# Kernel tuning notes

Measured on AMD Instinct MI355X. Metric: run time of the kernel, lower is better.

## Reference

```python
import jax, jax.numpy as jnp
import numpy as np

COST_CLASS, COST_BBOX, COST_GIOU = 2.0, 5.0, 2.0
ALPHA, GAMMA = 0.25, 2.0
EPS = 1e-8
N_CANDIDATE = 10


def box_cxcywh_to_xyxy(b):
    cx, cy, w, h = b[..., 0], b[..., 1], b[..., 2], b[..., 3]
    return jnp.stack([cx - 0.5 * w, cy - 0.5 * h, cx + 0.5 * w, cy + 0.5 * h], axis=-1)


def pairwise_iou_giou(b1, b2):
    # b1: [N,4] xyxy, b2: [M,4] xyxy -> iou [N,M], giou [N,M]
    area1 = (b1[:, 2] - b1[:, 0]) * (b1[:, 3] - b1[:, 1])
    area2 = (b2[:, 2] - b2[:, 0]) * (b2[:, 3] - b2[:, 1])
    lt = jnp.maximum(b1[:, None, :2], b2[None, :, :2])
    rb = jnp.minimum(b1[:, None, 2:], b2[None, :, 2:])
    wh = jnp.clip(rb - lt, 0.0)
    inter = wh[..., 0] * wh[..., 1]
    union = area1[:, None] + area2[None, :] - inter
    iou = inter / (union + EPS)
    # smallest enclosing box
    lt_c = jnp.minimum(b1[:, None, :2], b2[None, :, :2])
    rb_c = jnp.maximum(b1[:, None, 2:], b2[None, :, 2:])
    wh_c = jnp.clip(rb_c - lt_c, 0.0)
    area_c = wh_c[..., 0] * wh_c[..., 1]
    giou = iou - (area_c - union) / (area_c + EPS)
    return iou, giou


def _match_one(logits, boxes, labels, tboxes):
    # logits [Q,C], boxes [Q,4] cxcywh, labels [G] int, tboxes [G,4] cxcywh
    Q = logits.shape[0]
    G = labels.shape[0]
    prob = jax.nn.sigmoid(logits)                 # [Q,C]  (use_focal_loss path)
    p = prob[:, labels]                           # [Q,G] gather at GT classes
    neg_cost = (1.0 - ALPHA) * p ** GAMMA * (-jnp.log1p(-p + EPS))
    pos_cost = ALPHA * (1.0 - p) ** GAMMA * (-jnp.log(p + EPS))
    cost_class = pos_cost - neg_cost              # [Q,G]
    cost_bbox = jnp.sum(jnp.abs(boxes[:, None, :] - tboxes[None, :, :]), axis=-1)  # L1 cdist [Q,G]
    iou, giou = pairwise_iou_giou(box_cxcywh_to_xyxy(boxes), box_cxcywh_to_xyxy(tboxes))
    C = COST_BBOX * cost_bbox + COST_CLASS * cost_class + COST_GIOU * (-giou)      # [Q,G]

    # --- SimOTA matching (simota_matching), vectorized over GT ---
    cost = C.T                                    # [G,Q]
    ious = iou.T                                  # [G,Q]
    n_cand = min(N_CANDIDATE, Q)
    topk_ious, _ = jax.lax.top_k(ious, n_cand)    # [G,n_cand]
    dynamic_ks = jnp.clip(jnp.sum(topk_ious, axis=1).astype(jnp.int32), 1)  # [G]
    # rank of each anchor per GT under ascending cost
    ranks = jnp.argsort(jnp.argsort(cost, axis=1), axis=1)                  # [G,Q]
    matching = (ranks < dynamic_ks[:, None]).astype(cost.dtype)             # [G,Q]
    # resolve anchors matched to multiple GTs: keep argmin-cost GT
    anchor_matching_gt = matching.sum(axis=0)     # [Q]
    cost_argmin = jnp.argmin(cost, axis=0)        # [Q]
    onehot_min = (jnp.arange(G)[:, None] == cost_argmin[None, :]).astype(cost.dtype)
    matching = jnp.where(anchor_matching_gt[None, :] > 1, onehot_min, matching)
    return jnp.stack([cost, matching], axis=0)    # [2,G,Q]


def reference(pred_logits, pred_boxes, tgt_labels, tgt_boxes):
    # per-image cost blocks + SimOTA matching matrices: [bs, 2, G, Q]
    return jax.vmap(_match_one)(pred_logits, pred_boxes, tgt_labels, tgt_boxes)


def setup_inputs() -> dict:
    key = jax.random.key(0)
    k1, k2, k3, k4 = jax.random.split(key, 4)
    bs, Q, C, G = 16, 4000, 80, 128
    pred_logits = jax.random.normal(k1, (bs, Q, C), dtype=jnp.float32)
    pred_boxes = jax.random.uniform(k2, (bs, Q, 4), dtype=jnp.float32, minval=0.05, maxval=0.95)
    tgt_labels = jax.random.randint(k3, (bs, G), 0, C)
    tgt_boxes = jax.random.uniform(k4, (bs, G, 4), dtype=jnp.float32, minval=0.05, maxval=0.95)
    return {"pred_logits": pred_logits, "pred_boxes": pred_boxes,
            "tgt_labels": tgt_labels, "tgt_boxes": tgt_boxes}
```

## Files before the change

kernel.cpp:

```cpp
#include <hip/hip_runtime.h>
#include <cmath>
#include <cfloat>
#include <climits>


static constexpr int BS = 16;
static constexpr int Qn = 4000;
static constexpr int Cn = 80;
static constexpr int Gn = 128;
static constexpr float kEPS = 1e-8f;


static constexpr size_t kThrvOff = 0;
static constexpr size_t kThriOff = 8 * 1024;
static constexpr size_t kFOff    = 16 * 1024;
static constexpr size_t kFBytes  = (size_t)BS * Cn * Qn * sizeof(float);

__device__ __forceinline__ float focal_cost(float l) {
    const float p = 1.0f / (1.0f + expf(-l));
    const float neg = (0.75f * (p * p)) * (-log1pf(-p + kEPS));
    const float pos = (0.25f * ((1.0f - p) * (1.0f - p))) * (-logf(p + kEPS));
    return pos - neg;
}

__global__ __launch_bounds__(256) void kP_focal(
    const float* __restrict__ logits,
    float* __restrict__ F)
{
    const int b  = blockIdx.y;
    const int q0 = blockIdx.x * 32;
    const int t  = threadIdx.x;

    __shared__ float s_f[32 * 81];

    const float* src = logits + ((size_t)b * Qn + q0) * Cn;
#pragma unroll
    for (int i = 0; i < 10; ++i) {
        const int idx = t + i * 256;
        const int ql = idx / 80, c = idx % 80;
        s_f[ql * 81 + c] = focal_cost(src[idx]);
    }
    __syncthreads();

    float* dst = F + (size_t)b * Cn * Qn;
#pragma unroll
    for (int i = 0; i < 10; ++i) {
        const int j = t + i * 256;
        const int c = j >> 5, ql = j & 31;
        dst[(size_t)c * Qn + q0 + ql] = s_f[ql * 81 + c];
    }
}

__device__ __forceinline__ unsigned long long pack_ci(float c, int q) {
    const unsigned int u = __float_as_uint(c + 0.0f);
    const unsigned int s = (u & 0x80000000u) ? ~u : (u | 0x80000000u);
    return ((unsigned long long)s << 32) | (unsigned int)q;
}

__device__ __forceinline__ unsigned long long shfl_xor_u64(unsigned long long v, int m) {
    const int lo = __shfl_xor((int)(unsigned int)v, m, 64);
    const int hi = __shfl_xor((int)(unsigned int)(v >> 32), m, 64);
    return ((unsigned long long)(unsigned int)hi << 32) | (unsigned int)lo;
}

__device__ __forceinline__ unsigned long long bitonic64_asc_u64(unsigned long long v, int lane) {
#pragma unroll
    for (int k = 2; k <= 64; k <<= 1) {
#pragma unroll
        for (int j = 32; j >= 1; j >>= 1) {
            if (j < k) {
                const unsigned long long o = shfl_xor_u64(v, j);
                const bool up = ((lane & k) == 0);
                const bool keepmin = (((lane & j) == 0) == up);
                const bool omin = (o < v);
                v = (keepmin == omin) ? o : v;
            }
        }
    }
    return v;
}

__device__ __forceinline__ float bitonic64_asc_f32(float v, int lane) {
#pragma unroll
    for (int k = 2; k <= 64; k <<= 1) {
#pragma unroll
        for (int j = 32; j >= 1; j >>= 1) {
            if (j < k) {
                const float o = __shfl_xor(v, j, 64);
                const bool up = ((lane & k) == 0);
                const bool keepmin = (((lane & j) == 0) == up);
                const bool omin = (o < v);
                v = (keepmin == omin) ? o : v;
            }
        }
    }
    return v;
}

__device__ __forceinline__ void ins10_vi(float (&cv)[10], int (&ci)[10],
                                         float v, int q) {
    bool le[10];
#pragma unroll
    for (int j = 0; j < 10; ++j) le[j] = (cv[j] <= v);
#pragma unroll
    for (int j = 9; j >= 1; --j) {
        const float nv = le[j] ? cv[j] : (le[j - 1] ? v : cv[j - 1]);
        const int   ni = le[j] ? ci[j] : (le[j - 1] ? q : ci[j - 1]);
        cv[j] = nv; ci[j] = ni;
    }
    if (!le[0]) { cv[0] = v; ci[0] = q; }
}

__device__ __forceinline__ void ins10_desc(float (&iv)[10], float v) {
    bool ge[10];
#pragma unroll
    for (int j = 0; j < 10; ++j) ge[j] = (iv[j] >= v);
#pragma unroll
    for (int j = 9; j >= 1; --j)
        iv[j] = ge[j] ? iv[j] : (ge[j - 1] ? v : iv[j - 1]);
    if (!ge[0]) iv[0] = v;
}

template <bool USE_F>
__global__ __launch_bounds__(512, 8) void kF(
    const float* __restrict__ boxes,
    const int*   __restrict__ labels,
    const float* __restrict__ tboxes,
    const float* __restrict__ logits,
    const float* __restrict__ F,
    float* __restrict__ out,
    float* __restrict__ thrv,
    int*   __restrict__ thri)
{
    const int lane = threadIdx.x & 63;
    const int w8   = threadIdx.x >> 6;
    const int sub  = w8 & 3;
    const int r    = blockIdx.x;
    const int b    = r >> 7;
    const int g    = r & (Gn - 1);

    const float* tb = tboxes + (size_t)r * 4;
    const float tcx = tb[0], tcy = tb[1], tw = tb[2], th = tb[3];
    const float tx0 = tcx - 0.5f * tw, ty0 = tcy - 0.5f * th;
    const float tx1 = tcx + 0.5f * tw, ty1 = tcy + 0.5f * th;
    const float tarea = (tx1 - tx0) * (ty1 - ty0);

    const float4* brow = reinterpret_cast<const float4*>(boxes) + (size_t)b * Qn;

    __shared__ float              s_st[8][1024];
    __shared__ unsigned long long s_ccb[4][64];
    __shared__ float              s_icb[4][64];
    __shared__ int                s_cnt[8];
    __shared__ unsigned long long s_ce[4][12];
    __shared__ float              s_if[4][12];

    if (lane == 0) s_cnt[w8] = 0;

    if (w8 < 4) {
        const int lab = labels[r];
        const float* Frow = USE_F ? (F + ((size_t)b * Cn + lab) * Qn) : nullptr;
        const float* lcol = USE_F ? nullptr : (logits + (size_t)b * Qn * Cn + lab);
        float* crow = out + (size_t)(b * 2) * Gn * Qn + (size_t)g * Qn;

        float m0 = INFINITY;

#pragma unroll
        for (int it = 0; it < 4; ++it) {
            const int q0 = it * 1024 + sub * 256 + (lane << 2);
            if ((it < 3) || (q0 < Qn)) {
                float cls4[4];
                if (USE_F) {
                    const float4 f4 = *reinterpret_cast<const float4*>(Frow + q0);
                    cls4[0] = f4.x; cls4[1] = f4.y; cls4[2] = f4.z; cls4[3] = f4.w;
                } else {
#pragma unroll
                    for (int e = 0; e < 4; ++e)
                        cls4[e] = focal_cost(lcol[(size_t)(q0 + e) * Cn]);
                }
                float c4[4];
#pragma unroll
                for (int e = 0; e < 4; ++e) {
                    const float cls = cls4[e];
                    const float4 bb = brow[q0 + e];
                    const float cx = bb.x, cy = bb.y, w = bb.z, h = bb.w;
                    const float x0 = cx - 0.5f * w, y0 = cy - 0.5f * h;
                    const float x1 = cx + 0.5f * w, y1 = cy + 0.5f * h;
                    const float area1 = (x1 - x0) * (y1 - y0);
                    const float l1 = ((fabsf(cx - tcx) + fabsf(cy - tcy))
                                      + fabsf(w - tw)) + fabsf(h - th);
                    const float ltx = fmaxf(x0, tx0), lty = fmaxf(y0, ty0);
                    const float rbx = fminf(x1, tx1), rby = fminf(y1, ty1);
                    const float iw = fmaxf(rbx - ltx, 0.0f), ih = fmaxf(rby - lty, 0.0f);
                    const float inter = iw * ih;
                    const float uni = (area1 + tarea) - inter;
                    const float iou = inter / (uni + kEPS);
                    const float cltx = fminf(x0, tx0), clty = fminf(y0, ty0);
                    const float crbx = fmaxf(x1, tx1), crby = fmaxf(y1, ty1);
                    const float cw = fmaxf(crbx - cltx, 0.0f), ch = fmaxf(crby - clty, 0.0f);
                    const float areac = cw * ch;
                    const float giou = iou - (areac - uni) / (areac + kEPS);

                    const float cost = (5.0f * l1 + 2.0f * cls) + 2.0f * (-giou);
                    c4[e] = cost;
                    m0 = fminf(m0, cost);
                }
                float4 cv4; cv4.x = c4[0]; cv4.y = c4[1]; cv4.z = c4[2]; cv4.w = c4[3];
                *reinterpret_cast<float4*>(crow + q0) = cv4;
                *reinterpret_cast<float4*>(&s_st[w8][it * 256 + (lane << 2)]) = cv4;
            }
        }

        const float sorted = bitonic64_asc_f32(m0, lane);
        const float T = __shfl(sorted, 9, 64);

#pragma unroll
        for (int it = 0; it < 4; ++it) {
            const int q0 = it * 1024 + sub * 256 + (lane << 2);
            if ((it < 3) || (q0 < Qn)) {
                const float4 c4 = *reinterpret_cast<const float4*>(
                    &s_st[w8][it * 256 + (lane << 2)]);
#pragma unroll
                for (int e = 0; e < 4; ++e) {
                    const float c = (e == 0) ? c4.x : (e == 1) ? c4.y
                                  : (e == 2) ? c4.z : c4.w;
                    if (c <= T) {
                        const int slot = atomicAdd(&s_cnt[w8], 1);
                        if (slot < 64) s_ccb[sub][slot] = pack_ci(c, q0 + e);
                    }
                }
            }
        }

        const int cnt = s_cnt[w8];
        if (cnt <= 64) {
            unsigned long long v = (lane < cnt) ? s_ccb[sub][lane] : ~0ull;
            v = bitonic64_asc_u64(v, lane);
            if (lane < 12) s_ce[sub][lane] = (lane < 10) ? v : ~0ull;
        } else {
            float cv[10]; int ci[10];
#pragma unroll
            for (int j = 0; j < 10; ++j) { cv[j] = INFINITY; ci[j] = INT_MAX; }
#pragma unroll
            for (int it = 0; it < 4; ++it) {
                const int q0 = it * 1024 + sub * 256 + (lane << 2);
                if ((it < 3) || (q0 < Qn)) {
                    const float4 c4 = *reinterpret_cast<const float4*>(
                        &s_st[w8][it * 256 + (lane << 2)]);
                    ins10_vi(cv, ci, c4.x, q0);
                    ins10_vi(cv, ci, c4.y, q0 + 1);
                    ins10_vi(cv, ci, c4.z, q0 + 2);
                    ins10_vi(cv, ci, c4.w, q0 + 3);
                }
            }
#pragma unroll
            for (int t = 0; t < 10; ++t) {
                float m = cv[0];
#pragma unroll
                for (int d = 1; d <= 32; d <<= 1)
                    m = fminf(m, __shfl_xor(m, d, 64));
                int cq = (cv[0] == m) ? ci[0] : INT_MAX;
#pragma unroll
                for (int d = 1; d <= 32; d <<= 1)
                    cq = min(cq, __shfl_xor(cq, d, 64));
                if (lane == 0) s_ce[sub][t] = pack_ci(m, cq);
                const bool own = (cv[0] == m) && (ci[0] == cq);
                if (own) {
#pragma unroll
                    for (int j = 0; j < 9; ++j) { cv[j] = cv[j + 1]; ci[j] = ci[j + 1]; }
                    cv[9] = INFINITY; ci[9] = INT_MAX;
                }
            }
            if (lane < 2) s_ce[sub][10 + lane] = ~0ull;
        }
    } else {
        float M0 = -INFINITY;

#pragma unroll
        for (int it = 0; it < 4; ++it) {
            const int q0 = it * 1024 + sub * 256 + (lane << 2);
            if ((it < 3) || (q0 < Qn)) {
                float io4[4];
#pragma unroll
                for (int e = 0; e < 4; ++e) {
                    const float4 bb = brow[q0 + e];
                    const float x0 = bb.x - 0.5f * bb.z, y0 = bb.y - 0.5f * bb.w;
                    const float x1 = bb.x + 0.5f * bb.z, y1 = bb.y + 0.5f * bb.w;
                    const float area1 = (x1 - x0) * (y1 - y0);
                    const float ltx = fmaxf(x0, tx0), lty = fmaxf(y0, ty0);
                    const float rbx = fminf(x1, tx1), rby = fminf(y1, ty1);
                    const float iw = fmaxf(rbx - ltx, 0.0f), ih = fmaxf(rby - lty, 0.0f);
                    const float inter = iw * ih;
                    const float uni = (area1 + tarea) - inter;
                    const float iou = inter / (uni + kEPS);
                    io4[e] = iou;
                    M0 = fmaxf(M0, iou);
                }
                float4 iv4; iv4.x = io4[0]; iv4.y = io4[1]; iv4.z = io4[2]; iv4.w = io4[3];
                *reinterpret_cast<float4*>(&s_st[w8][it * 256 + (lane << 2)]) = iv4;
            }
        }

        const float sorted = bitonic64_asc_f32(M0, lane);
        const float T = __shfl(sorted, 54, 64);

#pragma unroll
        for (int it = 0; it < 4; ++it) {
            const int q0 = it * 1024 + sub * 256 + (lane << 2);
            if ((it < 3) || (q0 < Qn)) {
                const float4 c4 = *reinterpret_cast<const float4*>(
                    &s_st[w8][it * 256 + (lane << 2)]);
#pragma unroll
                for (int e = 0; e < 4; ++e) {
                    const float c = (e == 0) ? c4.x : (e == 1) ? c4.y
                                  : (e == 2) ? c4.z : c4.w;
                    if (c >= T) {
                        const int slot = atomicAdd(&s_cnt[w8], 1);
                        if (slot < 64) s_icb[sub][slot] = c;
                    }
                }
            }
        }

        const int cnt = s_cnt[w8];
        if (cnt <= 64) {
            float v = (lane < cnt) ? s_icb[sub][lane] : -INFINITY;
            v = bitonic64_asc_f32(v, lane);
            if (lane >= 54) s_if[sub][63 - lane] = v;
            if (lane < 2) s_if[sub][10 + lane] = -INFINITY;
        } else {
            float iv[10];
#pragma unroll
            for (int j = 0; j < 10; ++j) iv[j] = -INFINITY;
#pragma unroll
            for (int it = 0; it < 4; ++it) {
                const int q0 = it * 1024 + sub * 256 + (lane << 2);
                if ((it < 3) || (q0 < Qn)) {
                    const float4 c4 = *reinterpret_cast<const float4*>(
                        &s_st[w8][it * 256 + (lane << 2)]);
                    ins10_desc(iv, c4.x);
                    ins10_desc(iv, c4.y);
                    ins10_desc(iv, c4.z);
                    ins10_desc(iv, c4.w);
                }
            }
#pragma unroll
            for (int t = 0; t < 10; ++t) {
                float m = iv[0];
#pragma unroll
                for (int d = 1; d <= 32; d <<= 1)
                    m = fmaxf(m, __shfl_xor(m, d, 64));
                if (lane == 0) s_if[sub][t] = m;
                const bool own0 = (iv[0] == m);
                const unsigned long long bal = __ballot(own0);
                if (own0 && lane == __ffsll((long long)bal) - 1) {
#pragma unroll
                    for (int j = 0; j < 9; ++j) iv[j] = iv[j + 1];
                    iv[9] = -INFINITY;
                }
            }
            if (lane < 2) s_if[sub][10 + lane] = -INFINITY;
        }
    }

    __syncthreads();

    if (threadIdx.x == 0) {
        int p0 = 0, p1 = 0, p2 = 0, p3 = 0;
        float s = 0.0f;
#pragma unroll
        for (int t = 0; t < 10; ++t) {
            const float a0 = s_if[0][p0], a1 = s_if[1][p1];
            const float a2 = s_if[2][p2], a3 = s_if[3][p3];
            const float mx = fmaxf(fmaxf(a0, a1), fmaxf(a2, a3));
            if (a0 == mx) ++p0;
            else if (a1 == mx) ++p1;
            else if (a2 == mx) ++p2;
            else ++p3;
            s += mx;
        }
        int k = (int)s;
        if (k < 1) k = 1;
        if (k > 10) k = 10;

        p0 = 0; p1 = 0; p2 = 0; p3 = 0;
        unsigned long long key = 0;
#pragma unroll
        for (int t = 0; t < 10; ++t) {
            const unsigned long long a0 = s_ce[0][p0], a1 = s_ce[1][p1];
            const unsigned long long a2 = s_ce[2][p2], a3 = s_ce[3][p3];
            unsigned long long mn = a0;
            if (a1 < mn) mn = a1;
            if (a2 < mn) mn = a2;
            if (a3 < mn) mn = a3;
            if (a0 == mn) ++p0;
            else if (a1 == mn) ++p1;
            else if (a2 == mn) ++p2;
            else ++p3;
            if (t == k - 1) key = mn;
        }
        const unsigned int su = (unsigned int)(key >> 32);
        thrv[r] = __uint_as_float((su & 0x80000000u) ? (su ^ 0x80000000u) : ~su);
        thri[r] = (int)(unsigned int)key;
    }
}

__global__ __launch_bounds__(512) void kC5(
    const float* __restrict__ outc,
    const float* __restrict__ thrv,
    const int*   __restrict__ thri,
    float* __restrict__ out)
{
    const int b    = blockIdx.y;
    const int lane = threadIdx.x & 63;
    const int gh   = threadIdx.x >> 6;
    const int quad = blockIdx.x * 64 + lane;
    const int q0   = quad * 4;

    __shared__ float              s_tv[Gn];
    __shared__ int                s_ti[Gn];
    __shared__ unsigned long long s_mask[8][64];
    __shared__ float              s_mv0[8][64], s_mv1[8][64];
    __shared__ float              s_mv2[8][64], s_mv3[8][64];
    __shared__ unsigned           s_mg[8][64];

    if (threadIdx.x < Gn) {
        s_tv[threadIdx.x] = thrv[b * Gn + threadIdx.x];
        s_ti[threadIdx.x] = thri[b * Gn + threadIdx.x];
    }
    __syncthreads();

    const bool act = (quad < Qn / 4);
    const int gbase = gh * 16;
    unsigned long long mask = 0;
    float mv0 = INFINITY, mv1 = INFINITY, mv2 = INFINITY, mv3 = INFINITY;
    int mg0 = 0, mg1 = 0, mg2 = 0, mg3 = 0;

    if (act) {
        const float* crow = outc + (size_t)(b * 2) * Gn * Qn + q0;
#pragma unroll
        for (int j = 0; j < 16; ++j) {
            const int g = gbase + j;
            const float4 c = *reinterpret_cast<const float4*>(crow + (size_t)g * Qn);
            const float tvg = s_tv[g];
            const int   tig = s_ti[g];
            const bool t0 = (c.x < tvg) || (c.x == tvg && q0     <= tig);
            const bool t1 = (c.y < tvg) || (c.y == tvg && q0 + 1 <= tig);
            const bool t2 = (c.z < tvg) || (c.z == tvg && q0 + 2 <= tig);
            const bool t3 = (c.w < tvg) || (c.w == tvg && q0 + 3 <= tig);
            mask |= ((unsigned long long)t0 << j)
                  | ((unsigned long long)t1 << (16 + j))
                  | ((unsigned long long)t2 << (32 + j))
                  | ((unsigned long long)t3 << (48 + j));
            if (c.x < mv0) { mv0 = c.x; mg0 = g; }
            if (c.y < mv1) { mv1 = c.y; mg1 = g; }
            if (c.z < mv2) { mv2 = c.z; mg2 = g; }
            if (c.w < mv3) { mv3 = c.w; mg3 = g; }
        }
    }
    s_mask[gh][lane] = mask;
    s_mv0[gh][lane] = mv0; s_mv1[gh][lane] = mv1;
    s_mv2[gh][lane] = mv2; s_mv3[gh][lane] = mv3;
    s_mg[gh][lane] = (unsigned)mg0 | ((unsigned)mg1 << 8)
                   | ((unsigned)mg2 << 16) | ((unsigned)mg3 << 24);
    __syncthreads();

    int c0 = 0, c1 = 0, c2 = 0, c3 = 0;
#pragma unroll
    for (int h = 0; h < 8; ++h) {
        const unsigned long long m = s_mask[h][lane];
        c0 += __popcll(m & 0xFFFFull);
        c1 += __popcll((m >> 16) & 0xFFFFull);
        c2 += __popcll((m >> 32) & 0xFFFFull);
        c3 += __popcll((m >> 48) & 0xFFFFull);
    }
    float b0 = s_mv0[0][lane], b1 = s_mv1[0][lane];
    float b2 = s_mv2[0][lane], b3 = s_mv3[0][lane];
    unsigned pk = s_mg[0][lane];
    int g0b = pk & 0xFF, g1b = (pk >> 8) & 0xFF;
    int g2b = (pk >> 16) & 0xFF, g3b = (pk >> 24) & 0xFF;
#pragma unroll
    for (int h = 1; h < 8; ++h) {
        const unsigned pkh = s_mg[h][lane];
        const float v0 = s_mv0[h][lane];
        if (v0 < b0) { b0 = v0; g0b = pkh & 0xFF; }
        const float v1 = s_mv1[h][lane];
        if (v1 < b1) { b1 = v1; g1b = (pkh >> 8) & 0xFF; }
        const float v2 = s_mv2[h][lane];
        if (v2 < b2) { b2 = v2; g2b = (pkh >> 16) & 0xFF; }
        const float v3 = s_mv3[h][lane];
        if (v3 < b3) { b3 = v3; g3b = (pkh >> 24) & 0xFF; }
    }
    const bool f0 = (c0 > 1), f1 = (c1 > 1), f2 = (c2 > 1), f3 = (c3 > 1);

    if (act) {
        float* mrow = out + (size_t)(b * 2 + 1) * Gn * Qn + q0;
#pragma unroll
        for (int j = 0; j < 16; ++j) {
            const int g = gbase + j;
            float4 o;
            o.x = (f0 ? (g == g0b) : ((mask >> j) & 1ull))        ? 1.0f : 0.0f;
            o.y = (f1 ? (g == g1b) : ((mask >> (16 + j)) & 1ull)) ? 1.0f : 0.0f;
            o.z = (f2 ? (g == g2b) : ((mask >> (32 + j)) & 1ull)) ? 1.0f : 0.0f;
            o.w = (f3 ? (g == g3b) : ((mask >> (48 + j)) & 1ull)) ? 1.0f : 0.0f;
            *reinterpret_cast<float4*>(mrow + (size_t)g * Qn) = o;
        }
    }
}

extern "C" void kernel_launch(void* const* d_in, const int* in_sizes, int n_in,
                              void* d_out, int out_size, void* d_ws, size_t ws_size,
                              hipStream_t stream) {
    (void)in_sizes; (void)n_in; (void)out_size;
    const float* logits = (const float*)d_in[0];
    const float* boxes  = (const float*)d_in[1];
    const int*   labels = (const int*)d_in[2];
    const float* tboxes = (const float*)d_in[3];
    float* out = (float*)d_out;

    float* thrv = (float*)((char*)d_ws + kThrvOff);
    int*   thri = (int*)  ((char*)d_ws + kThriOff);
    float* F    = (float*)((char*)d_ws + kFOff);

    const bool use_f = (ws_size >= kFOff + kFBytes);

    dim3 gF(BS * Gn);
    if (use_f) {
        dim3 gP(Qn / 32, BS);
        kP_focal<<<gP, 256, 0, stream>>>(logits, F);
        kF<true><<<gF, 512, 0, stream>>>(boxes, labels, tboxes, logits, F,
                                         out, thrv, thri);
    } else {
        kF<false><<<gF, 512, 0, stream>>>(boxes, labels, tboxes, logits, nullptr,
                                          out, thrv, thri);
    }

    dim3 gC((Qn / 4 + 63) / 64, BS);
    kC5<<<gC, 512, 0, stream>>>(out, thrv, thri, out);
}
```

Before: 72.15 us.

## Share cost/IoU computation across all eight waves via shared memory

Previously waves 0-3 computed the cost row while waves 4-7 separately recomputed the IoU for every anchor, duplicating the box geometry work. Now all eight waves each compute a 512-anchor slice of both cost and IoU, write them to shared arrays, and derive per-wave thresholds that are combined through shared memory after a block barrier. This halves the per-thread geometry work and box loads, at the cost of a __syncthreads, a larger shared footprint (two 4096-float arrays), and looser combined thresholds that may admit more candidates into the fallback path.

Result: faster. 67.94 us (median of 2 runs) (-5.8%).

```diff
diff --git a/kernel.cpp b/kernel.cpp
--- a/kernel.cpp
+++ b/kernel.cpp
@@ -146,87 +146,100 @@
     const float tarea = (tx1 - tx0) * (ty1 - ty0);
 
     const float4* brow = reinterpret_cast<const float4*>(boxes) + (size_t)b * Qn;
-
-    __shared__ float              s_st[8][1024];
+    const int lab = labels[r];
+    const float* Frow = USE_F ? (F + ((size_t)b * Cn + lab) * Qn) : nullptr;
+    const float* lcol = USE_F ? nullptr : (logits + (size_t)b * Qn * Cn + lab);
+    float* crow = out + (size_t)(b * 2) * Gn * Qn + (size_t)g * Qn;
+
+    __shared__ float              s_cost[4096];
+    __shared__ float              s_iou[4096];
     __shared__ unsigned long long s_ccb[4][64];
     __shared__ float              s_icb[4][64];
     __shared__ int                s_cnt[8];
     __shared__ unsigned long long s_ce[4][12];
     __shared__ float              s_if[4][12];
+    __shared__ float              s_T[8];
 
     if (lane == 0) s_cnt[w8] = 0;
 
+    float trk = (w8 < 4) ? INFINITY : -INFINITY;
+
+#pragma unroll
+    for (int it = 0; it < 2; ++it) {
+        const int q0 = w8 * 512 + it * 256 + (lane << 2);
+        if ((it == 0) || (q0 < Qn)) {
+            float cls4[4];
+            if (USE_F) {
+                const float4 f4 = *reinterpret_cast<const float4*>(Frow + q0);
+                cls4[0] = f4.x; cls4[1] = f4.y; cls4[2] = f4.z; cls4[3] = f4.w;
+            } else {
+#pragma unroll
+                for (int e = 0; e < 4; ++e)
+                    cls4[e] = focal_cost(lcol[(size_t)(q0 + e) * Cn]);
+            }
+            float c4[4], io4[4];
+#pragma unroll
+            for (int e = 0; e < 4; ++e) {
+                const float cls = cls4[e];
+                const float4 bb = brow[q0 + e];
+                const float cx = bb.x, cy = bb.y, w = bb.z, h = bb.w;
+                const float x0 = cx - 0.5f * w, y0 = cy - 0.5f * h;
+                const float x1 = cx + 0.5f * w, y1 = cy + 0.5f * h;
+                const float area1 = (x1 - x0) * (y1 - y0);
+                const float l1 = ((fabsf(cx - tcx) + fabsf(cy - tcy))
+                                  + fabsf(w - tw)) + fabsf(h - th);
+                const float ltx = fmaxf(x0, tx0), lty = fmaxf(y0, ty0);
+                const float rbx = fminf(x1, tx1), rby = fminf(y1, ty1);
+                const float iw = fmaxf(rbx - ltx, 0.0f), ih = fmaxf(rby - lty, 0.0f);
+                const float inter = iw * ih;
+                const float uni = (area1 + tarea) - inter;
+                const float iou = inter / (uni + kEPS);
+                const float cltx = fminf(x0, tx0), clty = fminf(y0, ty0);
+                const float crbx = fmaxf(x1, tx1), crby = fmaxf(y1, ty1);
+                const float cw = fmaxf(crbx - cltx, 0.0f), ch = fmaxf(crby - clty, 0.0f);
+                const float areac = cw * ch;
+                const float giou = iou - (areac - uni) / (areac + kEPS);
+
+                const float cost = (5.0f * l1 + 2.0f * cls) + 2.0f * (-giou);
+                c4[e] = cost; io4[e] = iou;
+            }
+            if (w8 < 4) {
+                trk = fminf(trk, fminf(fminf(c4[0], c4[1]), fminf(c4[2], c4[3])));
+            } else {
+                trk = fmaxf(trk, fmaxf(fmaxf(io4[0], io4[1]), fmaxf(io4[2], io4[3])));
+            }
+            float4 cv4; cv4.x = c4[0]; cv4.y = c4[1]; cv4.z = c4[2]; cv4.w = c4[3];
+            float4 iv4; iv4.x = io4[0]; iv4.y = io4[1]; iv4.z = io4[2]; iv4.w = io4[3];
+            *reinterpret_cast<float4*>(crow + q0) = cv4;
+            *reinterpret_cast<float4*>(&s_cost[q0]) = cv4;
+            *reinterpret_cast<float4*>(&s_iou[q0]) = iv4;
+        } else {
+            float4 pi; pi.x = INFINITY; pi.y = INFINITY; pi.z = INFINITY; pi.w = INFINITY;
+            float4 ni; ni.x = -INFINITY; ni.y = -INFINITY; ni.z = -INFINITY; ni.w = -INFINITY;
+            *reinterpret_cast<float4*>(&s_cost[q0]) = pi;
+            *reinterpret_cast<float4*>(&s_iou[q0]) = ni;
+        }
+    }
+
+    const float sorted = bitonic64_asc_f32(trk, lane);
+    const float Tw = __shfl(sorted, (w8 < 4) ? 9 : 54, 64);
+    if (lane == 0) s_T[w8] = Tw;
+    __syncthreads();
+
     if (w8 < 4) {
-        const int lab = labels[r];
-        const float* Frow = USE_F ? (F + ((size_t)b * Cn + lab) * Qn) : nullptr;
-        const float* lcol = USE_F ? nullptr : (logits + (size_t)b * Qn * Cn + lab);
-        float* crow = out + (size_t)(b * 2) * Gn * Qn + (size_t)g * Qn;
-
-        float m0 = INFINITY;
-
+        const float T = fminf(fminf(s_T[0], s_T[1]), fminf(s_T[2], s_T[3]));
+        const int base = sub * 1024;
 #pragma unroll
         for (int it = 0; it < 4; ++it) {
-            const int q0 = it * 1024 + sub * 256 + (lane << 2);
-            if ((it < 3) || (q0 < Qn)) {
-                float cls4[4];
-                if (USE_F) {
-                    const float4 f4 = *reinterpret_cast<const float4*>(Frow + q0);
-                    cls4[0] = f4.x; cls4[1] = f4.y; cls4[2] = f4.z; cls4[3] = f4.w;
-                } else {
-#pragma unroll
-                    for (int e = 0; e < 4; ++e)
-                        cls4[e] = focal_cost(lcol[(size_t)(q0 + e) * Cn]);
-                }
-                float c4[4];
-#pragma unroll
-                for (int e = 0; e < 4; ++e) {
-                    const float cls = cls4[e];
-                    const float4 bb = brow[q0 + e];
-                    const float cx = bb.x, cy = bb.y, w = bb.z, h = bb.w;
-                    const float x0 = cx - 0.5f * w, y0 = cy - 0.5f * h;
-                    const float x1 = cx + 0.5f * w, y1 = cy + 0.5f * h;
-                    const float area1 = (x1 - x0) * (y1 - y0);
-                    const float l1 = ((fabsf(cx - tcx) + fabsf(cy - tcy))
-                                      + fabsf(w - tw)) + fabsf(h - th);
-                    const float ltx = fmaxf(x0, tx0), lty = fmaxf(y0, ty0);
-                    const float rbx = fminf(x1, tx1), rby = fminf(y1, ty1);
-                    const float iw = fmaxf(rbx - ltx, 0.0f), ih = fmaxf(rby - lty, 0.0f);
-                    const float inter = iw * ih;
-                    const float uni = (area1 + tarea) - inter;
-                    const float iou = inter / (uni + kEPS);
-                    const float cltx = fminf(x0, tx0), clty = fminf(y0, ty0);
-                    const float crbx = fmaxf(x1, tx1), crby = fmaxf(y1, ty1);
-                    const float cw = fmaxf(crbx - cltx, 0.0f), ch = fmaxf(crby - clty, 0.0f);
-                    const float areac = cw * ch;
-                    const float giou = iou - (areac - uni) / (areac + kEPS);
-
-                    const float cost = (5.0f * l1 + 2.0f * cls) + 2.0f * (-giou);
-                    c4[e] = cost;
-                    m0 = fminf(m0, cost);
-                }
-                float4 cv4; cv4.x = c4[0]; cv4.y = c4[1]; cv4.z = c4[2]; cv4.w = c4[3];
-                *reinterpret_cast<float4*>(crow + q0) = cv4;
-                *reinterpret_cast<float4*>(&s_st[w8][it * 256 + (lane << 2)]) = cv4;
-            }
-        }
-
-        const float sorted = bitonic64_asc_f32(m0, lane);
-        const float T = __shfl(sorted, 9, 64);
-
-#pragma unroll
-        for (int it = 0; it < 4; ++it) {
-            const int q0 = it * 1024 + sub * 256 + (lane << 2);
-            if ((it < 3) || (q0 < Qn)) {
-                const float4 c4 = *reinterpret_cast<const float4*>(
-                    &s_st[w8][it * 256 + (lane << 2)]);
-#pragma unroll
-                for (int e = 0; e < 4; ++e) {
-                    const float c = (e == 0) ? c4.x : (e == 1) ? c4.y
-                                  : (e == 2) ? c4.z : c4.w;
-                    if (c <= T) {
-                        const int slot = atomicAdd(&s_cnt[w8], 1);
-                        if (slot < 64) s_ccb[sub][slot] = pack_ci(c, q0 + e);
-                    }
+            const int idx = base + it * 256 + (lane << 2);
+            const float4 c4 = *reinterpret_cast<const float4*>(&s_cost[idx]);
+#pragma unroll
+            for (int e = 0; e < 4; ++e) {
+                const float c = (e == 0) ? c4.x : (e == 1) ? c4.y
+                              : (e == 2) ? c4.z : c4.w;
+                if (c <= T) {
+                    const int slot = atomicAdd(&s_cnt[w8], 1);
+                    if (slot < 64) s_ccb[sub][slot] = pack_ci(c, idx + e);
                 }
             }
         }
@@ -242,15 +255,12 @@
             for (int j = 0; j < 10; ++j) { cv[j] = INFINITY; ci[j] = INT_MAX; }
 #pragma unroll
             for (int it = 0; it < 4; ++it) {
-                const int q0 = it * 1024 + sub * 256 + (lane << 2);
-                if ((it < 3) || (q0 < Qn)) {
-                    const float4 c4 = *reinterpret_cast<const float4*>(
-                        &s_st[w8][it * 256 + (lane << 2)]);
-                    ins10_vi(cv, ci, c4.x, q0);
-                    ins10_vi(cv, ci, c4.y, q0 + 1);
-                    ins10_vi(cv, ci, c4.z, q0 + 2);
-                    ins10_vi(cv, ci, c4.w, q0 + 3);
-                }
+                const int idx = base + it * 256 + (lane << 2);
+                const float4 c4 = *reinterpret_cast<const float4*>(&s_cost[idx]);
+                ins10_vi(cv, ci, c4.x, idx);
+                ins10_vi(cv, ci, c4.y, idx + 1);
+                ins10_vi(cv, ci, c4.z, idx + 2);
+                ins10_vi(cv, ci, c4.w, idx + 3);
             }
 #pragma unroll
             for (int t = 0; t < 10; ++t) {
@@ -273,50 +283,19 @@
             if (lane < 2) s_ce[sub][10 + lane] = ~0ull;
         }
     } else {
-        float M0 = -INFINITY;
-
+        const float T = fmaxf(fmaxf(s_T[4], s_T[5]), fmaxf(s_T[6], s_T[7]));
+        const int base = sub * 1024;
 #pragma unroll
         for (int it = 0; it < 4; ++it) {
-            const int q0 = it * 1024 + sub * 256 + (lane << 2);
-            if ((it < 3) || (q0 < Qn)) {
-                float io4[4];
-#pragma unroll
-                for (int e = 0; e < 4; ++e) {
-                    const float4 bb = brow[q0 + e];
-                    const float x0 = bb.x - 0.5f * bb.z, y0 = bb.y - 0.5f * bb.w;
-                    const float x1 = bb.x + 0.5f * bb.z, y1 = bb.y + 0.5f * bb.w;
-                    const float area1 = (x1 - x0) * (y1 - y0);
-                    const float ltx = fmaxf(x0, tx0), lty = fmaxf(y0, ty0);
-                    const float rbx = fminf(x1, tx1), rby = fminf(y1, ty1);
-                    const float iw = fmaxf(rbx - ltx, 0.0f), ih = fmaxf(rby - lty, 0.0f);
-                    const float inter = iw * ih;
-                    const float uni = (area1 + tarea) - inter;
-                    const float iou = inter / (uni + kEPS);
-                    io4[e] = iou;
-                    M0 = fmaxf(M0, iou);
-                }
-                float4 iv4; iv4.x = io4[0]; iv4.y = io4[1]; iv4.z = io4[2]; iv4.w = io4[3];
-                *reinterpret_cast<float4*>(&s_st[w8][it * 256 + (lane << 2)]) = iv4;
-            }
-        }
-
-        const float sorted = bitonic64_asc_f32(M0, lane);
-        const float T = __shfl(sorted, 54, 64);
-
-#pragma unroll
-        for (int it = 0; it < 4; ++it) {
-            const int q0 = it * 1024 + sub * 256 + (lane << 2);
-            if ((it < 3) || (q0 < Qn)) {
-                const float4 c4 = *reinterpret_cast<const float4*>(
-                    &s_st[w8][it * 256 + (lane << 2)]);
-#pragma unroll
-                for (int e = 0; e < 4; ++e) {
-                    const float c = (e == 0) ? c4.x : (e == 1) ? c4.y
-                                  : (e == 2) ? c4.z : c4.w;
-                    if (c >= T) {
-                        const int slot = atomicAdd(&s_cnt[w8], 1);
-                        if (slot < 64) s_icb[sub][slot] = c;
-                    }
+            const int idx = base + it * 256 + (lane << 2);
+            const float4 i4 = *reinterpret_cast<const float4*>(&s_iou[idx]);
+#pragma unroll
+            for (int e = 0; e < 4; ++e) {
+                const float v = (e == 0) ? i4.x : (e == 1) ? i4.y
+                              : (e == 2) ? i4.z : i4.w;
+                if (v >= T) {
+                    const int slot = atomicAdd(&s_cnt[w8], 1);
+                    if (slot < 64) s_icb[sub][slot] = v;
                 }
             }
         }
@@ -333,15 +312,12 @@
             for (int j = 0; j < 10; ++j) iv[j] = -INFINITY;
 #pragma unroll
             for (int it = 0; it < 4; ++it) {
-                const int q0 = it * 1024 + sub * 256 + (lane << 2);
-                if ((it < 3) || (q0 < Qn)) {
-                    const float4 c4 = *reinterpret_cast<const float4*>(
-                        &s_st[w8][it * 256 + (lane << 2)]);
-                    ins10_desc(iv, c4.x);
-                    ins10_desc(iv, c4.y);
-                    ins10_desc(iv, c4.z);
-                    ins10_desc(iv, c4.w);
-                }
+                const int idx = base + it * 256 + (lane << 2);
+                const float4 i4 = *reinterpret_cast<const float4*>(&s_iou[idx]);
+                ins10_desc(iv, i4.x);
+                ins10_desc(iv, i4.y);
+                ins10_desc(iv, i4.z);
+                ins10_desc(iv, i4.w);
             }
 #pragma unroll
             for (int t = 0; t < 10; ++t) {
```
